# Kernel tuning notes

Measured on AMD Instinct MI355X. Metric: run time of the kernel, lower is better.

The kernel has to match this reference:

```python
import jax, jax.numpy as jnp
import numpy as np

HN, ND, STRIDE, ESTRIDE = 10, 40, 3, 3  # hidden_node, ndim, stride, encode_stride


def _build_graphs():
    # Dense aggregation matrices A[dst, src] equivalent to the module's fixed
    # edge lists (scatter-add of src features into dst). Graph is tiny (10/40
    # nodes) and identical across the batch, so dense matmul is the efficient
    # exact form of the gather->scatter-add.
    w = np.float32(np.exp(-(1.0 / STRIDE) ** 2))
    A_pred = np.zeros((HN, HN), np.float32)
    for j in range(HN):
        A_pred[j, j] += 1.0                      # edge [j, j], weight 1
        for dj in range(1, STRIDE - 1):          # dj = 1 only
            A_pred[(j - dj) % HN, j] += w        # edge [j, j-dj]
            A_pred[(j + dj) % HN, j] += w        # edge [j, j+dj]
    A_enc = np.zeros((HN, ND), np.float32)
    A_dec = np.zeros((ND, HN), np.float32)
    for j in range(HN):
        cg = (j * ND // HN) % ND                 # center_grid = 4j
        for i in range(cg - ESTRIDE, cg + ESTRIDE):
            A_enc[j, i % ND] += 1.0              # grid i -> hidden j
            A_dec[i % ND, j] += 1.0              # hidden j -> grid i
    return jnp.asarray(A_enc), jnp.asarray(A_pred), jnp.asarray(A_dec)

A_ENC, A_PRED, A_DEC = _build_graphs()


def setup_inputs() -> dict:
    key = jax.random.key(0)
    ks = jax.random.split(key, 12)
    B, HF = 524288, 8
    s = 0.3  # modest weight scale
    return {
        "x": jax.random.normal(ks[0], (B, ND), jnp.float32),
        "z": jax.random.uniform(ks[1], (B, HN, HF), dtype=jnp.float32),
        "y": jax.random.uniform(ks[2], (B, ND, 1), dtype=jnp.float32),
        "enc_rel_w": jax.random.normal(ks[3], (HF, 1), jnp.float32) * s,
        "enc_rel_b": jax.random.normal(ks[4], (HF,), jnp.float32) * s,
        "enc_root_w": jax.random.normal(ks[5], (HF, HF), jnp.float32) * s,
        "pred_rel_w": jax.random.normal(ks[6], (HF, HF), jnp.float32) * s,
        "pred_rel_b": jax.random.normal(ks[7], (HF,), jnp.float32) * s,
        "pred_root_w": jax.random.normal(ks[8], (HF, HF), jnp.float32) * s,
        "dec_rel_w": jax.random.normal(ks[9], (1, HF), jnp.float32) * s,
        "dec_rel_b": jax.random.normal(ks[10], (1,), jnp.float32) * s,
        "dec_root_w": jax.random.normal(ks[11], (1, 1), jnp.float32) * s,
    }


def reference(x, z, y, enc_rel_w, enc_rel_b, enc_root_w,
              pred_rel_w, pred_rel_b, pred_root_w,
              dec_rel_w, dec_rel_b, dec_root_w):
    xb = x[..., None]  # [B, 40, 1]
    # encoder GraphConv((1, 8) -> 8): lin_rel(agg(x_src)) + lin_root(z)
    agg = jnp.einsum('ds,bsf->bdf', A_ENC, xb)                 # [B, 10, 1]
    z1 = jax.nn.relu(agg @ enc_rel_w.T + enc_rel_b + z @ enc_root_w.T)
    # predictor GraphConv(8 -> 8) with edge weights folded into A_PRED
    agg2 = jnp.einsum('ds,bsf->bdf', A_PRED, z1)               # [B, 10, 8]
    z2 = jax.nn.relu(agg2 @ pred_rel_w.T + pred_rel_b + z1 @ pred_root_w.T)
    # decoder GraphConv((8, 1) -> 1)
    agg3 = jnp.einsum('ds,bsf->bdf', A_DEC, z2)                # [B, 40, 8]
    out = agg3 @ dec_rel_w.T + dec_rel_b + y @ dec_root_w.T   # [B, 40, 1]
    return out[..., 0]                                         # [B, 40]
```

## Files before the change

kernel.cpp:

```cpp
#include <hip/hip_runtime.h>


#define HN 10
#define ND 40
#define HF 8
#define TPB 256
#define WLEN 64
#define ROW4 11
#define ZROW 5

__global__ __launch_bounds__(TPB) void gnn_kernel(
    const float* __restrict__ x,
    const float* __restrict__ z,
    const float* __restrict__ y,
    const float* __restrict__ enc_rel_w,
    const float* __restrict__ enc_rel_b,
    const float* __restrict__ enc_root_w,
    const float* __restrict__ pred_rel_w,
    const float* __restrict__ pred_rel_b,
    const float* __restrict__ pred_root_w,
    const float* __restrict__ dec_rel_w,
    const float* __restrict__ dec_rel_b,
    const float* __restrict__ dec_root_w,
    float* __restrict__ out,
    int B)
{
    __shared__ float4 lds4[TPB * ROW4];
    const int t  = threadIdx.x;
    const int l  = t & 63;
    const int wv = t >> 6;
    const long long W = (long long)blockIdx.x * TPB + wv * WLEN;
    float4* wl = lds4 + wv * (WLEN * ROW4);

    const float w = 0.8948393168143698f;

    const float4* xg4 = (const float4*)x;
    const float4* zg4 = (const float4*)z;
    const float4* yg4 = (const float4*)y;
    float4*       og4 = (float4*)out;

    const float drb   = dec_rel_b[0];
    const float droot = dec_root_w[0];

    auto enc_row = [&](float aggv, float4 v0, float4 v1, float (&r)[HF]) {
        float zrow[HF] = {v0.x, v0.y, v0.z, v0.w, v1.x, v1.y, v1.z, v1.w};
        #pragma unroll
        for (int f = 0; f < HF; ++f) {
            float acc = aggv * enc_rel_w[f] + enc_rel_b[f];
            #pragma unroll
            for (int g = 0; g < HF; ++g)
                acc += zrow[g] * enc_root_w[f * HF + g];
            r[f] = fmaxf(acc, 0.0f);
        }
    };

    auto emit = [&](const float (&rm)[HF], const float (&rc)[HF],
                    const float (&rp)[HF]) -> float {
        float a2[HF];
        #pragma unroll
        for (int f = 0; f < HF; ++f)
            a2[f] = rc[f] + w * (rm[f] + rp[f]);
        float s = 0.0f;
        #pragma unroll
        for (int f = 0; f < HF; ++f) {
            float acc = pred_rel_b[f];
            #pragma unroll
            for (int g = 0; g < HF; ++g)
                acc += a2[g] * pred_rel_w[f * HF + g];
            #pragma unroll
            for (int g = 0; g < HF; ++g)
                acc += rc[g] * pred_root_w[f * HF + g];
            s += fmaxf(acc, 0.0f) * dec_rel_w[f];
        }
        return s;
    };

    const long long xw = W * 10 + l;
    #pragma unroll
    for (int k = 0; k < 10; ++k) {
        int i = l + 64 * k; int r = i / 10, q = i - r * 10;
        wl[r * ROW4 + q] = xg4[W * 10 + i];
    }
    const int  zbr = l >> 2, zm = l & 3;
    const long long zb = (W + zbr) * 20 + zm;
    float4 zt0 = zg4[zb +   0];
    float4 zt1 = zg4[zb + 320];
    float4 zt2 = zg4[zb + 640];
    float4 zt3 = zg4[zb + 960];
    asm volatile("s_waitcnt lgkmcnt(0)" ::: "memory");
    __builtin_amdgcn_sched_barrier(0);

    float a_[10];
    {
        float4 prev = wl[l * ROW4 + 9];
        #pragma unroll
        for (int k = 0; k < 10; ++k) {
            float4 cur = wl[l * ROW4 + k];
            a_[k] = prev.y + prev.z + prev.w + cur.x + cur.y + cur.z;
            prev = cur;
        }
    }
    float u0 = a_[2], u1 = a_[3], u2 = a_[4], u3 = a_[5],
          u4 = a_[6], u5 = a_[7], u6 = a_[8], u7 = a_[9];

    wl[(zbr +  0) * ZROW + zm] = zt0;
    wl[(zbr + 16) * ZROW + zm] = zt1;
    wl[(zbr + 32) * ZROW + zm] = zt2;
    wl[(zbr + 48) * ZROW + zm] = zt3;
    zt0 = zg4[zb +   0 + 4];
    zt1 = zg4[zb + 320 + 4];
    zt2 = zg4[zb + 640 + 4];
    zt3 = zg4[zb + 960 + 4];
    asm volatile("s_waitcnt lgkmcnt(0)" ::: "memory");
    __builtin_amdgcn_sched_barrier(0);
    float r0s[HF], r1s[HF];
    {
        float4 q0 = wl[l * ZROW + 0], q1 = wl[l * ZROW + 1],
               q2 = wl[l * ZROW + 2], q3 = wl[l * ZROW + 3];
        enc_row(a_[0], q0, q1, r0s);
        enc_row(a_[1], q2, q3, r1s);
    }
    float rm[HF], rc[HF];
    #pragma unroll
    for (int f = 0; f < HF; ++f) { rm[f] = r0s[f]; rc[f] = r1s[f]; }

    float t0 = 0.f, t1 = 0.f, t2 = 0.f, t3 = 0.f,
          t4 = 0.f, t5 = 0.f, t6 = 0.f, t7 = 0.f;

    #pragma unroll 1
    for (int j = 1; j <= 4; ++j) {
        float4* bw = wl + (j & 1) * (WLEN * ZROW);
        bw[(zbr +  0) * ZROW + zm] = zt0;
        bw[(zbr + 16) * ZROW + zm] = zt1;
        bw[(zbr + 32) * ZROW + zm] = zt2;
        bw[(zbr + 48) * ZROW + zm] = zt3;
        if (j < 4) {
            zt0 = zg4[zb +   0 + 4 * (j + 1)];
            zt1 = zg4[zb + 320 + 4 * (j + 1)];
            zt2 = zg4[zb + 640 + 4 * (j + 1)];
            zt3 = zg4[zb + 960 + 4 * (j + 1)];
        }
        asm volatile("s_waitcnt lgkmcnt(0)" ::: "memory");
        __builtin_amdgcn_sched_barrier(0);
        float4 q0 = bw[l * ZROW + 0], q1 = bw[l * ZROW + 1],
               q2 = bw[l * ZROW + 2], q3 = bw[l * ZROW + 3];

        float rp0[HF], rp1[HF];
        enc_row(u0, q0, q1, rp0);
        enc_row(u1, q2, q3, rp1);
        const float sA = emit(rm, rc, rp0);
        const float sB = emit(rc, rp0, rp1);

        t0 = t2; t1 = t3; t2 = t4; t3 = t5; t4 = t6; t5 = t7;
        t6 = sA; t7 = sB;
        u0 = u2; u1 = u3; u2 = u4; u3 = u5; u4 = u6; u5 = u7;
        #pragma unroll
        for (int f = 0; f < HF; ++f) { rm[f] = rp0[f]; rc[f] = rp1[f]; }
    }

    float4 Y0 = yg4[xw +   0], Y1 = yg4[xw +  64], Y2 = yg4[xw + 128],
           Y3 = yg4[xw + 192], Y4 = yg4[xw + 256], Y5 = yg4[xw + 320],
           Y6 = yg4[xw + 384], Y7 = yg4[xw + 448], Y8 = yg4[xw + 512],
           Y9 = yg4[xw + 576];

    const float s9 = emit(rm, rc, r0s);
    const float s0 = emit(rc, r0s, r1s);

    auto stage_pair = [&](int k, float sa, float sb) {
        const float pair = sa + sb + drb;
        float4 vo;
        vo.x = sa + drb;
        vo.y = pair;
        vo.z = pair;
        vo.w = sb + drb;
        wl[l * ROW4 + k] = vo;
    };
    stage_pair(0, s0, t0);
    stage_pair(1, t0, t1);
    stage_pair(2, t1, t2);
    stage_pair(3, t2, t3);
    stage_pair(4, t3, t4);
    stage_pair(5, t4, t5);
    stage_pair(6, t5, t6);
    stage_pair(7, t6, t7);
    stage_pair(8, t7, s9);
    stage_pair(9, s9, s0);
    asm volatile("s_waitcnt lgkmcnt(0)" ::: "memory");
    __builtin_amdgcn_sched_barrier(0);

    auto drain = [&](int k, float4 vy) {
        int i = l + 64 * k; int r = i / 10, q = i - r * 10;
        float4 p = wl[r * ROW4 + q];
        p.x += vy.x * droot;
        p.y += vy.y * droot;
        p.z += vy.z * droot;
        p.w += vy.w * droot;
        og4[W * 10 + i] = p;
    };
    drain(0, Y0); drain(1, Y1); drain(2, Y2); drain(3, Y3); drain(4, Y4);
    drain(5, Y5); drain(6, Y6); drain(7, Y7); drain(8, Y8); drain(9, Y9);
}

extern "C" void kernel_launch(void* const* d_in, const int* in_sizes, int n_in,
                              void* d_out, int out_size, void* d_ws, size_t ws_size,
                              hipStream_t stream) {
    const float* x          = (const float*)d_in[0];
    const float* z          = (const float*)d_in[1];
    const float* y          = (const float*)d_in[2];
    const float* enc_rel_w  = (const float*)d_in[3];
    const float* enc_rel_b  = (const float*)d_in[4];
    const float* enc_root_w = (const float*)d_in[5];
    const float* pred_rel_w = (const float*)d_in[6];
    const float* pred_rel_b = (const float*)d_in[7];
    const float* pred_root_w= (const float*)d_in[8];
    const float* dec_rel_w  = (const float*)d_in[9];
    const float* dec_rel_b  = (const float*)d_in[10];
    const float* dec_root_w = (const float*)d_in[11];
    float* out = (float*)d_out;

    const int B = in_sizes[0] / ND;
    const int blocks = B / TPB;
    gnn_kernel<<<blocks, TPB, 0, stream>>>(
        x, z, y, enc_rel_w, enc_rel_b, enc_root_w,
        pred_rel_w, pred_rel_b, pred_root_w,
        dec_rel_w, dec_rel_b, dec_root_w, out, B);
}
```

Before: 373.2 us.

## Issue all x and z global loads upfront via inline asm with staged vmcnt waits

Replaces the per-iteration z prefetch and the upfront x loads with 30 inline-asm global_load_dwordx4 issued at kernel start, followed by explicit vmcnt waits that release each z chunk as it is consumed. The loop is fully unrolled into macro steps. The aim is to keep many more memory requests in flight per wave in this bandwidth-bound kernel. In exchange it raises VGPR pressure by about 120 registers, which may lower occupancy. It also relies on inline-asm loads whose ordering the compiler cannot track, so correctness depends on the manual vmcnt counts and on no compiler-generated loads being interleaved.

```diff
diff --git a/kernel.cpp b/kernel.cpp
--- a/kernel.cpp
+++ b/kernel.cpp
@@ -8,6 +8,15 @@
 #define WLEN 64
 #define ROW4 11
 #define ZROW 5
+
+#define GLD(dst, addr) \
+    asm volatile("global_load_dwordx4 %0, %1, off" : "=v"(dst) : "v"(addr))
+#define VMWAIT(n) do { \
+    asm volatile("s_waitcnt vmcnt(" #n ")"); \
+    __builtin_amdgcn_sched_barrier(0); } while (0)
+#define LGKM0() do { \
+    asm volatile("s_waitcnt lgkmcnt(0)" ::: "memory"); \
+    __builtin_amdgcn_sched_barrier(0); } while (0)
 
 __global__ __launch_bounds__(TPB) void gnn_kernel(
     const float* __restrict__ x,
@@ -39,6 +48,29 @@
     const float4* yg4 = (const float4*)y;
     float4*       og4 = (float4*)out;
 
+    const long long xw = W * 10 + l;
+    float4 X0, X1, X2, X3, X4, X5, X6, X7, X8, X9;
+    GLD(X0, xg4 + xw +   0); GLD(X1, xg4 + xw +  64);
+    GLD(X2, xg4 + xw + 128); GLD(X3, xg4 + xw + 192);
+    GLD(X4, xg4 + xw + 256); GLD(X5, xg4 + xw + 320);
+    GLD(X6, xg4 + xw + 384); GLD(X7, xg4 + xw + 448);
+    GLD(X8, xg4 + xw + 512); GLD(X9, xg4 + xw + 576);
+
+    const int  zbr = l >> 2, zm = l & 3;
+    const long long zb = (W + zbr) * 20 + zm;
+    float4 ZA0, ZA1, ZA2, ZA3, ZB0, ZB1, ZB2, ZB3, ZC0, ZC1, ZC2, ZC3,
+           ZD0, ZD1, ZD2, ZD3, ZE0, ZE1, ZE2, ZE3;
+    GLD(ZA0, zg4 + zb +   0 +  0); GLD(ZA1, zg4 + zb + 320 +  0);
+    GLD(ZA2, zg4 + zb + 640 +  0); GLD(ZA3, zg4 + zb + 960 +  0);
+    GLD(ZB0, zg4 + zb +   0 +  4); GLD(ZB1, zg4 + zb + 320 +  4);
+    GLD(ZB2, zg4 + zb + 640 +  4); GLD(ZB3, zg4 + zb + 960 +  4);
+    GLD(ZC0, zg4 + zb +   0 +  8); GLD(ZC1, zg4 + zb + 320 +  8);
+    GLD(ZC2, zg4 + zb + 640 +  8); GLD(ZC3, zg4 + zb + 960 +  8);
+    GLD(ZD0, zg4 + zb +   0 + 12); GLD(ZD1, zg4 + zb + 320 + 12);
+    GLD(ZD2, zg4 + zb + 640 + 12); GLD(ZD3, zg4 + zb + 960 + 12);
+    GLD(ZE0, zg4 + zb +   0 + 16); GLD(ZE1, zg4 + zb + 320 + 16);
+    GLD(ZE2, zg4 + zb + 640 + 16); GLD(ZE3, zg4 + zb + 960 + 16);
+
     const float drb   = dec_rel_b[0];
     const float droot = dec_root_w[0];
 
@@ -75,20 +107,16 @@
         return s;
     };
 
-    const long long xw = W * 10 + l;
-    #pragma unroll
-    for (int k = 0; k < 10; ++k) {
-        int i = l + 64 * k; int r = i / 10, q = i - r * 10;
-        wl[r * ROW4 + q] = xg4[W * 10 + i];
+    VMWAIT(20);
+    {
+        auto put = [&](int k, float4 v) {
+            int i = l + 64 * k; int r = i / 10, q = i - r * 10;
+            wl[r * ROW4 + q] = v;
+        };
+        put(0, X0); put(1, X1); put(2, X2); put(3, X3); put(4, X4);
+        put(5, X5); put(6, X6); put(7, X7); put(8, X8); put(9, X9);
     }
-    const int  zbr = l >> 2, zm = l & 3;
-    const long long zb = (W + zbr) * 20 + zm;
-    float4 zt0 = zg4[zb +   0];
-    float4 zt1 = zg4[zb + 320];
-    float4 zt2 = zg4[zb + 640];
-    float4 zt3 = zg4[zb + 960];
-    asm volatile("s_waitcnt lgkmcnt(0)" ::: "memory");
-    __builtin_amdgcn_sched_barrier(0);
+    LGKM0();
 
     float a_[10];
     {
@@ -103,16 +131,12 @@
     float u0 = a_[2], u1 = a_[3], u2 = a_[4], u3 = a_[5],
           u4 = a_[6], u5 = a_[7], u6 = a_[8], u7 = a_[9];
 
-    wl[(zbr +  0) * ZROW + zm] = zt0;
-    wl[(zbr + 16) * ZROW + zm] = zt1;
-    wl[(zbr + 32) * ZROW + zm] = zt2;
-    wl[(zbr + 48) * ZROW + zm] = zt3;
-    zt0 = zg4[zb +   0 + 4];
-    zt1 = zg4[zb + 320 + 4];
-    zt2 = zg4[zb + 640 + 4];
-    zt3 = zg4[zb + 960 + 4];
-    asm volatile("s_waitcnt lgkmcnt(0)" ::: "memory");
-    __builtin_amdgcn_sched_barrier(0);
+    VMWAIT(16);
+    wl[(zbr +  0) * ZROW + zm] = ZA0;
+    wl[(zbr + 16) * ZROW + zm] = ZA1;
+    wl[(zbr + 32) * ZROW + zm] = ZA2;
+    wl[(zbr + 48) * ZROW + zm] = ZA3;
+    LGKM0();
     float r0s[HF], r1s[HF];
     {
         float4 q0 = wl[l * ZROW + 0], q1 = wl[l * ZROW + 1],
@@ -127,36 +151,34 @@
     float t0 = 0.f, t1 = 0.f, t2 = 0.f, t3 = 0.f,
           t4 = 0.f, t5 = 0.f, t6 = 0.f, t7 = 0.f;
 
-    #pragma unroll 1
-    for (int j = 1; j <= 4; ++j) {
-        float4* bw = wl + (j & 1) * (WLEN * ZROW);
-        bw[(zbr +  0) * ZROW + zm] = zt0;
-        bw[(zbr + 16) * ZROW + zm] = zt1;
-        bw[(zbr + 32) * ZROW + zm] = zt2;
-        bw[(zbr + 48) * ZROW + zm] = zt3;
-        if (j < 4) {
-            zt0 = zg4[zb +   0 + 4 * (j + 1)];
-            zt1 = zg4[zb + 320 + 4 * (j + 1)];
-            zt2 = zg4[zb + 640 + 4 * (j + 1)];
-            zt3 = zg4[zb + 960 + 4 * (j + 1)];
-        }
-        asm volatile("s_waitcnt lgkmcnt(0)" ::: "memory");
-        __builtin_amdgcn_sched_barrier(0);
-        float4 q0 = bw[l * ZROW + 0], q1 = bw[l * ZROW + 1],
-               q2 = bw[l * ZROW + 2], q3 = bw[l * ZROW + 3];
-
-        float rp0[HF], rp1[HF];
-        enc_row(u0, q0, q1, rp0);
-        enc_row(u1, q2, q3, rp1);
-        const float sA = emit(rm, rc, rp0);
-        const float sB = emit(rc, rp0, rp1);
-
-        t0 = t2; t1 = t3; t2 = t4; t3 = t5; t4 = t6; t5 = t7;
-        t6 = sA; t7 = sB;
-        u0 = u2; u1 = u3; u2 = u4; u3 = u5; u4 = u6; u5 = u7;
-        #pragma unroll
-        for (int f = 0; f < HF; ++f) { rm[f] = rp0[f]; rc[f] = rp1[f]; }
-    }
+    #define ZSTEP(N, G0, G1, G2, G3, BUFOFF)                                \
+    do {                                                                    \
+        VMWAIT(N);                                                          \
+        float4* bw = wl + (BUFOFF);                                         \
+        bw[(zbr +  0) * ZROW + zm] = G0;                                    \
+        bw[(zbr + 16) * ZROW + zm] = G1;                                    \
+        bw[(zbr + 32) * ZROW + zm] = G2;                                    \
+        bw[(zbr + 48) * ZROW + zm] = G3;                                    \
+        LGKM0();                                                            \
+        float4 q0 = bw[l * ZROW + 0], q1 = bw[l * ZROW + 1],                \
+               q2 = bw[l * ZROW + 2], q3 = bw[l * ZROW + 3];                \
+        float rp0[HF], rp1[HF];                                             \
+        enc_row(u0, q0, q1, rp0);                                           \
+        enc_row(u1, q2, q3, rp1);                                           \
+        const float sA = emit(rm, rc, rp0);                                 \
+        const float sB = emit(rc, rp0, rp1);                                \
+        t0 = t2; t1 = t3; t2 = t4; t3 = t5; t4 = t6; t5 = t7;               \
+        t6 = sA; t7 = sB;                                                   \
+        u0 = u2; u1 = u3; u2 = u4; u3 = u5; u4 = u6; u5 = u7;               \
+        _Pragma("unroll")                                                   \
+        for (int f = 0; f < HF; ++f) { rm[f] = rp0[f]; rc[f] = rp1[f]; }    \
+    } while (0)
+
+    ZSTEP(12, ZB0, ZB1, ZB2, ZB3, WLEN * ZROW);
+    ZSTEP( 8, ZC0, ZC1, ZC2, ZC3, 0);
+    ZSTEP( 4, ZD0, ZD1, ZD2, ZD3, WLEN * ZROW);
+    ZSTEP( 0, ZE0, ZE1, ZE2, ZE3, 0);
+    #undef ZSTEP
 
     float4 Y0 = yg4[xw +   0], Y1 = yg4[xw +  64], Y2 = yg4[xw + 128],
            Y3 = yg4[xw + 192], Y4 = yg4[xw + 256], Y5 = yg4[xw + 320],
@@ -185,8 +207,7 @@
     stage_pair(7, t6, t7);
     stage_pair(8, t7, s9);
     stage_pair(9, s9, s0);
-    asm volatile("s_waitcnt lgkmcnt(0)" ::: "memory");
-    __builtin_amdgcn_sched_barrier(0);
+    LGKM0();
 
     auto drain = [&](int k, float4 vy) {
         int i = l + 64 * k; int r = i / 10, q = i - r * 10;
```

Result: no change. 377.8 us (+1.3%).
